# Kernel tuning notes

Measured on AMD Instinct MI355X. Metric: run time of the kernel, lower is better.

The kernel has to match this reference:

```python
import jax, jax.numpy as jnp
import numpy as np


def setup_inputs() -> dict:
    key = jax.random.key(0)
    ks = jax.random.split(key, 16)
    N, F_in, C, E = 50000, 128, 64, 800000
    H = 2 * C      # hidden width of first GCN layer = 128
    P = 128        # num_proj_hidden
    K = 3          # cluster_num (hardcoded in GRACE)

    def lin(kw, fan_in, fan_out):
        # torch Linear default init: U(-1/sqrt(fan_in), 1/sqrt(fan_in))
        bound = 1.0 / np.sqrt(fan_in)
        return jax.random.uniform(kw, (fan_in, fan_out), jnp.float32, -bound, bound)

    inp = {
        "x1": jax.random.normal(ks[0], (N, F_in), jnp.float32),
        "edge_index1": jax.random.randint(ks[1], (2, E), 0, N, jnp.int64 if jax.config.jax_enable_x64 else jnp.int32),
        "x2": jax.random.normal(ks[2], (N, F_in), jnp.float32),
        "edge_index2": jax.random.randint(ks[3], (2, E), 0, N, jnp.int64 if jax.config.jax_enable_x64 else jnp.int32),
        # encoder GCN layers
        "W1": lin(ks[4], F_in, H), "b1": jnp.zeros((H,), jnp.float32),
        "W2": lin(ks[5], H, C),    "b2": jnp.zeros((C,), jnp.float32),
        # instance projector: Linear(C,C) -> ReLU -> Linear(C,P)
        "Wp1": lin(ks[6], C, C), "bp1": jnp.zeros((C,), jnp.float32),
        "Wp2": lin(ks[7], C, P), "bp2": jnp.zeros((P,), jnp.float32),
        # cluster projector: Linear(C,C) -> ReLU -> Linear(C,K) -> Softmax
        "Wc1": lin(ks[8], C, C), "bc1": jnp.zeros((C,), jnp.float32),
        "Wc2": lin(ks[9], C, K), "bc2": jnp.zeros((K,), jnp.float32),
    }
    return inp


def _gcn_encoder(x, edge_index, W1, b1, W2, b2):
    N = x.shape[0]
    loop = jnp.arange(N, dtype=edge_index.dtype)
    row = jnp.concatenate([edge_index[0], loop])  # message sources (x_j)
    col = jnp.concatenate([edge_index[1], loop])  # aggregation targets
    deg = jax.ops.segment_sum(jnp.ones_like(col, jnp.float32), col, num_segments=N)
    dinv = jax.lax.rsqrt(deg)  # deg >= 1 due to self loops
    norm = dinv[row] * dinv[col]  # [E+N]

    def layer(h, W, b):
        h = h @ W  # transform first (PyG GCNConv), [N, F_out]
        msg = h[row] * norm[:, None]  # gather + scale, [E+N, F_out]
        return jax.ops.segment_sum(msg, col, num_segments=N) + b

    h = jax.nn.relu(layer(x, W1, b1))
    h = jax.nn.relu(layer(h, W2, b2))
    return h


def _l2norm(z, eps=1e-12):
    # matches F.normalize(z, dim=1): x / max(||x||, eps)
    n = jnp.sqrt(jnp.sum(z * z, axis=1, keepdims=True))
    return z / jnp.maximum(n, eps)


def reference(x1, edge_index1, x2, edge_index2,
              W1, b1, W2, b2, Wp1, bp1, Wp2, bp2, Wc1, bc1, Wc2, bc2):
    z1 = _gcn_encoder(x1, edge_index1, W1, b1, W2, b2)
    z2 = _gcn_encoder(x2, edge_index2, W1, b1, W2, b2)

    inst = lambda z: _l2norm(jax.nn.relu(z @ Wp1 + bp1) @ Wp2 + bp2)
    clus = lambda z: jax.nn.softmax(jax.nn.relu(z @ Wc1 + bc1) @ Wc2 + bc2, axis=1)

    z_i = inst(z1)
    z_j = inst(z2)
    c_i = clus(z1)
    c_j = clus(z2)
    return (z_i, z_j, c_i, c_j)
```

## Files before the change

### kernel.cpp

```cpp
#include <hip/hip_runtime.h>
#include <cstdint>
#include <cstddef>

using u16 = unsigned short;
using u32 = unsigned int;

typedef __bf16 bf16x8 __attribute__((ext_vector_type(8)));
typedef float  f32x4  __attribute__((ext_vector_type(4)));

__device__ __forceinline__ float bf2f(u16 b) { union { u32 i; float f; } v; v.i = ((u32)b) << 16; return v.f; }
__device__ __forceinline__ u16 f2bf(float f) { __bf16 b = (__bf16)f; return __builtin_bit_cast(u16, b); }
__device__ __forceinline__ float bflo(u32 u) { union { u32 i; float f; } v; v.i = u << 16; return v.f; }
__device__ __forceinline__ float bfhi(u32 u) { union { u32 i; float f; } v; v.i = u & 0xffff0000u; return v.f; }
__device__ __forceinline__ u32 pack2(float a, float b) { return (u32)f2bf(a) | ((u32)f2bf(b) << 16); }

__device__ __forceinline__ float loadx(const void* p, size_t i, int flag_bf16) {
    return flag_bf16 ? bf2f(((const u16*)p)[i]) : ((const float*)p)[i];
}
__device__ __forceinline__ void storex(void* p, size_t i, float v, int flag_bf16) {
    if (flag_bf16) ((u16*)p)[i] = f2bf(v);
    else           ((float*)p)[i] = v;
}

__device__ __forceinline__ bf16x8 load_afrag_ext(const void* A, size_t off, int flag) {
    if (flag) return *reinterpret_cast<const bf16x8*>((const u16*)A + off);
    const float* f = (const float*)A + off;
    float4 a = *reinterpret_cast<const float4*>(f);
    float4 b = *reinterpret_cast<const float4*>(f + 4);
    bf16x8 r;
    r[0] = (__bf16)a.x; r[1] = (__bf16)a.y; r[2] = (__bf16)a.z; r[3] = (__bf16)a.w;
    r[4] = (__bf16)b.x; r[5] = (__bf16)b.y; r[6] = (__bf16)b.z; r[7] = (__bf16)b.w;
    return r;
}

__global__ void k_detect(const u32* __restrict__ x, int* __restrict__ flag) {
    int lane = threadIdx.x;
    u32 u = x[lane];
    int e = (u >> 7) & 0xFF;
    int hit = (e >= 100 && e <= 145) ? 1 : 0;
    unsigned long long b = __ballot(hit);
    if (lane == 0) flag[0] = (__popcll(b) >= 32) ? 1 : 0;
}

struct ConvJob { const void* src; float* dst; int n; };
struct ConvJobs { ConvJob j[12]; };

__global__ void k_wconv(ConvJobs jobs, const int* __restrict__ flagp) {
    const int f = *flagp;
    const int stride = gridDim.x * blockDim.x;
    for (int s = 0; s < 12; ++s) {
        const ConvJob jb = jobs.j[s];
        for (int i = blockIdx.x * blockDim.x + threadIdx.x; i < jb.n; i += stride)
            jb.dst[i] = loadx(jb.src, i, f);
    }
}

struct TJob { const float* W; u16* WT; int K, NC; };
struct TJobs { TJob j[5]; };

__global__ void k_wtrans(TJobs jobs) {
    const int stride = gridDim.x * blockDim.x;
    for (int s = 0; s < 5; ++s) {
        const TJob jb = jobs.j[s];
        const int tot = jb.K * jb.NC;
        for (int i = blockIdx.x * blockDim.x + threadIdx.x; i < tot; i += stride) {
            int k = i / jb.NC, n = i - k * jb.NC;
            jb.WT[n * jb.K + k] = f2bf(jb.W[i]);
        }
    }
}

static const int CAPSH = 12;
static const int OVCAP = 65536;

__global__ __launch_bounds__(256) void k_bin(const int* __restrict__ ei0, const int* __restrict__ ei1,
                                             int* __restrict__ cur, u32* __restrict__ stage,
                                             int2* __restrict__ ov, int* __restrict__ ocnt,
                                             int E, int NB, int nblk) {
    const int g = blockIdx.y;
    const int* ei = g ? ei1 : ei0;
    const int chunk = (E + nblk - 1) / nblk;
    const int e0 = blockIdx.x * chunk;
    const int e1 = (e0 + chunk < E) ? e0 + chunk : E;
    const int tid = threadIdx.x;
    __shared__ int h[512];
    __shared__ int lb[512];
    for (int i = tid; i < NB; i += 256) h[i] = 0;
    __syncthreads();
    for (int e = e0 + tid; e < e1; e += 256) {
        int d = __builtin_nontemporal_load(ei + E + e);
        atomicAdd(&h[d >> 7], 1);
    }
    __syncthreads();
    for (int b = tid; b < NB; b += 256) {
        int c = h[b];
        lb[b] = c ? atomicAdd(&cur[g * NB + b], c) : 0;
    }
    __syncthreads();
    for (int i = tid; i < NB; i += 256) h[i] = 0;
    __syncthreads();
    for (int e = e0 + tid; e < e1; e += 256) {
        int s = __builtin_nontemporal_load(ei + e);
        int d = ei[E + e];
        int b = d >> 7;
        int p = lb[b] + atomicAdd(&h[b], 1);
        if (p < (1 << CAPSH)) {
            stage[((size_t)(g * NB + b) << CAPSH) + p] = (u32)s | ((u32)(d & 127) << 16);
        } else {
            int oi = atomicAdd(ocnt, 1);
            if (oi < OVCAP) ov[oi] = make_int2(s, d | (g << 24));
        }
    }
}

__global__ __launch_bounds__(256) void k_bscan(const int* __restrict__ cur, const int2* __restrict__ ov,
                                               const int* __restrict__ ocnt, int* __restrict__ bbase,
                                               int* __restrict__ rowptr, int N, int E, int NB) {
    __shared__ int tot[2][512];
    const int tid = threadIdx.x;
    for (int g = 0; g < 2; ++g)
        for (int i = tid; i < 512; i += 256) {
            int s = 0;
            if (i < NB) {
                int cv = cur[g * NB + i];
                s = (cv < (1 << CAPSH)) ? cv : (1 << CAPSH);
            }
            tot[g][i] = s;
        }
    __syncthreads();
    int no = *ocnt; if (no > OVCAP) no = OVCAP;
    for (int i = tid; i < no; i += 256) {
        int y = ov[i].y;
        atomicAdd(&tot[y >> 24][(y & 0xFFFFFF) >> 7], 1);
    }
    __syncthreads();
    int o00 = tot[0][tid], o01 = tot[0][tid + 256];
    int o10 = tot[1][tid], o11 = tot[1][tid + 256];
    for (int off = 1; off < 512; off <<= 1) {
        int a0 = tot[0][tid]       + ((tid >= off)       ? tot[0][tid - off]       : 0);
        int a1 = tot[0][tid + 256] + ((tid + 256 >= off) ? tot[0][tid + 256 - off] : 0);
        int b0 = tot[1][tid]       + ((tid >= off)       ? tot[1][tid - off]       : 0);
        int b1 = tot[1][tid + 256] + ((tid + 256 >= off) ? tot[1][tid + 256 - off] : 0);
        __syncthreads();
        tot[0][tid] = a0; tot[0][tid + 256] = a1;
        tot[1][tid] = b0; tot[1][tid + 256] = b1;
        __syncthreads();
    }
    if (tid < NB)       { bbase[tid]            = tot[0][tid] - o00;       bbase[NB + tid]       = tot[1][tid] - o10; }
    if (tid + 256 < NB) { bbase[tid + 256]      = tot[0][tid + 256] - o01; bbase[NB + tid + 256] = tot[1][tid + 256] - o11; }
    if (tid == 0) {
        rowptr[N] = E;
        rowptr[(size_t)(N + 1) + N] = E;
    }
}

__global__ __launch_bounds__(256) void k_scatter(const int* __restrict__ cur, const u32* __restrict__ stage,
                                                 const int2* __restrict__ ov, const int* __restrict__ ocnt,
                                                 const int* __restrict__ bbase, int* __restrict__ rowptr,
                                                 float* __restrict__ dinv, int* __restrict__ csr,
                                                 int N, int E, int NB) {
    const int g = blockIdx.y, b = blockIdx.x, tid = threadIdx.x;
    const int lo = b << 7;
    int R = N - lo; if (R > 128) R = 128;
    __shared__ int hist[128], scn[128], curs[128];
    if (tid < 128) hist[tid] = 0;
    __syncthreads();
    int cv = cur[g * NB + b];
    const int n = (cv < (1 << CAPSH)) ? cv : (1 << CAPSH);
    const u32* sp = stage + ((size_t)(g * NB + b) << CAPSH);
    for (int i = tid; i < n; i += 256) atomicAdd(&hist[sp[i] >> 16], 1);
    int no = *ocnt; if (no > OVCAP) no = OVCAP;
    for (int i = tid; i < no; i += 256) {
        int y = ov[i].y;
        if ((y >> 24) != g) continue;
        int d = y & 0xFFFFFF;
        if (d >= lo && d < lo + 128) atomicAdd(&hist[d - lo], 1);
    }
    __syncthreads();
    int orig = (tid < 128) ? hist[tid] : 0;
    if (tid < 128) scn[tid] = orig;
    __syncthreads();
    for (int off = 1; off < 128; off <<= 1) {
        int v = 0;
        if (tid < 128) v = scn[tid] + ((tid >= off) ? scn[tid - off] : 0);
        __syncthreads();
        if (tid < 128) scn[tid] = v;
        __syncthreads();
    }
    const int base = bbase[g * NB + b];
    if (tid < R) {
        int ex = base + scn[tid] - orig;
        rowptr[(size_t)g * (N + 1) + lo + tid] = ex;
        curs[tid] = ex;
        dinv[(size_t)g * N + lo + tid] = rsqrtf((float)(orig + 1));
    }
    __syncthreads();
    int* out = csr + (size_t)g * E;
    for (int i = tid; i < n; i += 256) {
        u32 v = sp[i];
        int pos = atomicAdd(&curs[v >> 16], 1);
        out[pos] = (int)(v & 0xFFFFu);
    }
    for (int i = tid; i < no; i += 256) {
        int y = ov[i].y;
        if ((y >> 24) != g) continue;
        int d = y & 0xFFFFFF;
        if (d >= lo && d < lo + 128) {
            int pos = atomicAdd(&curs[d - lo], 1);
            out[pos] = ov[i].x;
        }
    }
}

template <int K, int NC, bool AEXT, bool BIAS, bool RELU, bool NORM, bool OEXT, bool SCALE>
__global__ __launch_bounds__(256) void k_mgemm(const void* __restrict__ A0, const void* __restrict__ A1,
                                               size_t astride, const u16* __restrict__ WT,
                                               const float* __restrict__ bias, void* __restrict__ outv,
                                               size_t out_off, size_t ostride, int M,
                                               const int* __restrict__ flagp,
                                               const float* __restrict__ dvp) {
    constexpr int NT = NC / 16;
    constexpr int KI = K / 32;
    const int flag = *flagp;
    const int g = blockIdx.y;
    const void* Av = g ? A1 : A0;
    const int lane = threadIdx.x & 63;
    const int wave = threadIdx.x >> 6;
    const int q = lane >> 4;
    const int c = lane & 15;
    const int m0 = blockIdx.x * 64 + wave * 16;
    int arow = m0 + c;
    if (arow > M - 1) arow = M - 1;
    const size_t abase = (size_t)g * astride + (size_t)arow * K;

    bf16x8 afr[KI];
#pragma unroll
    for (int ki = 0; ki < KI; ++ki) {
        size_t off = abase + (size_t)ki * 32 + q * 8;
        if (AEXT) afr[ki] = load_afrag_ext(Av, off, flag);
        else      afr[ki] = *reinterpret_cast<const bf16x8*>((const u16*)Av + off);
    }

    f32x4 acc[NT];
#pragma unroll
    for (int t = 0; t < NT; ++t) acc[t] = (f32x4){0.f, 0.f, 0.f, 0.f};

#pragma unroll
    for (int ki = 0; ki < KI; ++ki) {
#pragma unroll
        for (int t = 0; t < NT; ++t) {
            const u16* bptr = WT + (size_t)(t * 16 + c) * K + ki * 32 + q * 8;
            bf16x8 bfr = *reinterpret_cast<const bf16x8*>(bptr);
            acc[t] = __builtin_amdgcn_mfma_f32_16x16x32_bf16(afr[ki], bfr, acc[t], 0, 0, 0);
        }
    }

#pragma unroll
    for (int t = 0; t < NT; ++t) {
        float bv = BIAS ? bias[t * 16 + c] : 0.f;
#pragma unroll
        for (int r = 0; r < 4; ++r) {
            float v = acc[t][r] + bv;
            if (RELU) v = fmaxf(v, 0.f);
            acc[t][r] = v;
        }
    }

    if constexpr (NORM) {
        float ss[4] = {0.f, 0.f, 0.f, 0.f};
#pragma unroll
        for (int t = 0; t < NT; ++t)
#pragma unroll
            for (int r = 0; r < 4; ++r) ss[r] += acc[t][r] * acc[t][r];
#pragma unroll
        for (int r = 0; r < 4; ++r) {
#pragma unroll
            for (int m = 1; m < 16; m <<= 1) ss[r] += __shfl_xor(ss[r], m, 64);
            float s = 1.f / fmaxf(sqrtf(ss[r]), 1e-12f);
#pragma unroll
            for (int t = 0; t < NT; ++t) acc[t][r] *= s;
        }
    }

    const size_t obase = out_off + (size_t)g * ostride;
#pragma unroll
    for (int r = 0; r < 4; ++r) {
        const int grow = m0 + q * 4 + r;
        if (grow < M) {
            float sc = 1.f;
            if constexpr (SCALE) sc = dvp[(size_t)g * M + grow];
#pragma unroll
            for (int t = 0; t < NT; ++t) {
                float v = SCALE ? acc[t][r] * sc : acc[t][r];
                size_t oi = obase + (size_t)grow * NC + t * 16 + c;
                if (OEXT) storex(outv, oi, v, flag);
                else      ((u16*)outv)[oi] = f2bf(v);
            }
        }
    }
}

__global__ __launch_bounds__(256) void k_agg128(const u32* __restrict__ H, const int* __restrict__ rowptr,
                                                const int* __restrict__ csr, const float* __restrict__ dinv,
                                                const float* __restrict__ bias, u32* __restrict__ out,
                                                int N, int E) {
    const int g = blockIdx.y;
    const int node = blockIdx.x * 4 + (threadIdx.x >> 6);
    if (node >= N) return;
    const int lane = threadIdx.x & 63;
    const u32* h = H + (size_t)g * N * 64;
    const int* rp = rowptr + (size_t)g * (N + 1);
    const int* cs = csr + (size_t)g * E;
    const float dn = dinv[(size_t)g * N + node];
    int e = rp[node];
    const int end = rp[node + 1];
    u32 su = h[(size_t)node * 64 + lane];
    float a0 = bflo(su), a1 = bfhi(su);
    while (e < end) {
        int cnt = end - e; if (cnt > 64) cnt = 64;
        int my = (lane < cnt) ? cs[e + lane] : 0;
        int j = 0;
        for (; j + 8 <= cnt; j += 8) {
            int sx[8];
#pragma unroll
            for (int k = 0; k < 8; ++k) sx[k] = __shfl(my, j + k, 64);
            u32 hv[8];
#pragma unroll
            for (int k = 0; k < 8; ++k) hv[k] = h[(size_t)sx[k] * 64 + lane];
#pragma unroll
            for (int k = 0; k < 8; ++k) { a0 += bflo(hv[k]); a1 += bfhi(hv[k]); }
        }
        for (; j < cnt; ++j) {
            int s = __shfl(my, j, 64);
            u32 hv = h[(size_t)s * 64 + lane];
            a0 += bflo(hv); a1 += bfhi(hv);
        }
        e += cnt;
    }
    a0 = fmaxf(a0 * dn + bias[2 * lane], 0.f);
    a1 = fmaxf(a1 * dn + bias[2 * lane + 1], 0.f);
    out[((size_t)g * N + node) * 64 + lane] = pack2(a0, a1);
}

__global__ __launch_bounds__(256) void k_agg64(const u16* __restrict__ H, const int* __restrict__ rowptr,
                                               const int* __restrict__ csr, const float* __restrict__ dinv,
                                               const float* __restrict__ bias, u16* __restrict__ out,
                                               int N, int E) {
    const int g = blockIdx.y;
    const int node = blockIdx.x * 4 + (threadIdx.x >> 6);
    if (node >= N) return;
    const int lane = threadIdx.x & 63;
    const u16* h = H + (size_t)g * N * 64;
    const int* rp = rowptr + (size_t)g * (N + 1);
    const int* cs = csr + (size_t)g * E;
    const float dn = dinv[(size_t)g * N + node];
    int e = rp[node];
    const int end = rp[node + 1];
    float a0 = bf2f(h[(size_t)node * 64 + lane]);
    while (e < end) {
        int cnt = end - e; if (cnt > 64) cnt = 64;
        int my = (lane < cnt) ? cs[e + lane] : 0;
        int j = 0;
        for (; j + 8 <= cnt; j += 8) {
            int sx[8];
#pragma unroll
            for (int k = 0; k < 8; ++k) sx[k] = __shfl(my, j + k, 64);
            u16 hv[8];
#pragma unroll
            for (int k = 0; k < 8; ++k) hv[k] = h[(size_t)sx[k] * 64 + lane];
#pragma unroll
            for (int k = 0; k < 8; ++k) a0 += bf2f(hv[k]);
        }
        for (; j < cnt; ++j) {
            int s = __shfl(my, j, 64);
            a0 += bf2f(h[(size_t)s * 64 + lane]);
        }
        e += cnt;
    }
    a0 = fmaxf(a0 * dn + bias[lane], 0.f);
    out[((size_t)g * N + node) * 64 + lane] = f2bf(a0);
}

__global__ __launch_bounds__(256) void k_clus(const u16* __restrict__ v, const float* __restrict__ Wc2,
                                              const float* __restrict__ bc2, void* __restrict__ outv,
                                              size_t out_off, size_t ostride, int N,
                                              const int* __restrict__ flagp) {
    const int g = blockIdx.y;
    const int node = blockIdx.x * 4 + (threadIdx.x >> 6);
    if (node >= N) return;
    const int flag = *flagp;
    const int lane = threadIdx.x & 63;
    float ul = bf2f(v[((size_t)g * N + node) * 64 + lane]);
    float a0 = ul * Wc2[lane * 3 + 0];
    float a1 = ul * Wc2[lane * 3 + 1];
    float a2 = ul * Wc2[lane * 3 + 2];
#pragma unroll
    for (int m = 1; m < 64; m <<= 1) {
        a0 += __shfl_xor(a0, m, 64);
        a1 += __shfl_xor(a1, m, 64);
        a2 += __shfl_xor(a2, m, 64);
    }
    a0 += bc2[0]; a1 += bc2[1]; a2 += bc2[2];
    float mx = fmaxf(a0, fmaxf(a1, a2));
    float e0 = expf(a0 - mx), e1 = expf(a1 - mx), e2 = expf(a2 - mx);
    float inv = 1.f / (e0 + e1 + e2);
    if (lane < 3) {
        float r = (lane == 0) ? e0 : ((lane == 1) ? e1 : e2);
        storex(outv, out_off + (size_t)g * ostride + (size_t)node * 3 + lane, r * inv, flag);
    }
}

extern "C" void kernel_launch(void* const* d_in, const int* in_sizes, int n_in,
                              void* d_out, int out_size, void* d_ws, size_t ws_size,
                              hipStream_t stream) {
    const int N = in_sizes[0] / 128;
    const int E = in_sizes[1] / 2;
    const int* ei0 = (const int*)d_in[1];
    const int* ei1 = (const int*)d_in[3];
    const int NB = (N + 127) >> 7;

    size_t off = 0;
    auto alloc = [&](size_t bytes) -> void* {
        void* p = (char*)d_ws + off;
        off += (bytes + 255) & ~(size_t)255;
        return p;
    };
    int* flag = (int*)alloc(256);
    const int wcnt[12] = {128 * 128, 128, 128 * 64, 64, 64 * 64, 64, 64 * 128, 128, 64 * 64, 64, 64 * 3, 3};
    float* wf[12];
    for (int i = 0; i < 12; ++i) wf[i] = (float*)alloc((size_t)wcnt[i] * 4);
    float* b1f = wf[1]; float* b2f = wf[3]; float* bp1f = wf[5]; float* bp2f = wf[7];
    float* bc1f = wf[9]; float* Wc2f = wf[10]; float* bc2f = wf[11];
    u16* W1T  = (u16*)alloc(128 * 128 * 2);
    u16* W2T  = (u16*)alloc(64 * 128 * 2);
    u16* Wp1T = (u16*)alloc(64 * 64 * 2);
    u16* Wp2T = (u16*)alloc(128 * 64 * 2);
    u16* Wc1T = (u16*)alloc(64 * 64 * 2);

    const int ncell = 2 * NB;
    int* cur    = (int*)alloc((size_t)(ncell + 1) * 4);
    int* ocnt   = cur + ncell;
    int2* ov    = (int2*)alloc((size_t)OVCAP * 8);
    u32* stage  = (u32*)alloc(((size_t)ncell << CAPSH) * 4);
    int* bbase  = (int*)alloc((size_t)2 * NB * 4);
    int* rowptr = (int*)alloc((size_t)2 * (N + 1) * 4);
    float* dinv = (float*)alloc((size_t)2 * N * 4);
    int* csr    = (int*)alloc((size_t)2 * E * 4);
    u16* A1 = (u16*)alloc((size_t)2 * N * 128 * 2);
    u16* H2 = A1;
    u16* Qb = (u16*)alloc((size_t)2 * N * 128 * 2);
    u16* U  = Qb;
    u16* Z  = (u16*)alloc((size_t)2 * N * 64 * 2);
    (void)ws_size; (void)n_in; (void)out_size;

    k_detect<<<1, 64, 0, stream>>>((const u32*)d_in[0], flag);
    ConvJobs jobs;
    for (int i = 0; i < 12; ++i) jobs.j[i] = ConvJob{d_in[4 + i], wf[i], wcnt[i]};
    k_wconv<<<64, 256, 0, stream>>>(jobs, flag);
    TJobs tj;
    tj.j[0] = TJob{wf[0], W1T, 128, 128};
    tj.j[1] = TJob{wf[2], W2T, 128, 64};
    tj.j[2] = TJob{wf[4], Wp1T, 64, 64};
    tj.j[3] = TJob{wf[6], Wp2T, 64, 128};
    tj.j[4] = TJob{wf[8], Wc1T, 64, 64};
    k_wtrans<<<40, 256, 0, stream>>>(tj);

    hipMemsetAsync(cur, 0, (size_t)(ncell + 1) * 4, stream);
    const int NBLK = 128;
    k_bin<<<dim3(NBLK, 2), 256, 0, stream>>>(ei0, ei1, cur, stage, ov, ocnt, E, NB, NBLK);
    k_bscan<<<1, 256, 0, stream>>>(cur, ov, ocnt, bbase, rowptr, N, E, NB);
    k_scatter<<<dim3(NB, 2), 256, 0, stream>>>(cur, stage, ov, ocnt, bbase, rowptr, dinv, csr, N, E, NB);

    const dim3 gM((N + 63) / 64, 2);
    const dim3 gA((N + 3) / 4, 2);

    k_mgemm<128, 128, true, false, false, false, false, true><<<gM, 256, 0, stream>>>(
        d_in[0], d_in[2], 0, W1T, nullptr, A1, 0, (size_t)N * 128, N, flag, dinv);
    k_agg128<<<gA, 256, 0, stream>>>((const u32*)A1, rowptr, csr, dinv, b1f, (u32*)Qb, N, E);
    k_mgemm<128, 64, false, false, false, false, false, true><<<gM, 256, 0, stream>>>(
        Qb, Qb, (size_t)N * 128, W2T, nullptr, H2, 0, (size_t)N * 64, N, flag, dinv);
    k_agg64<<<gA, 256, 0, stream>>>(H2, rowptr, csr, dinv, b2f, Z, N, E);

    k_mgemm<64, 64, false, true, true, false, false, false><<<gM, 256, 0, stream>>>(
        Z, Z, (size_t)N * 64, Wp1T, bp1f, U, 0, (size_t)N * 64, N, flag, nullptr);
    k_mgemm<64, 128, false, true, false, true, true, false><<<gM, 256, 0, stream>>>(
        U, U, (size_t)N * 64, Wp2T, bp2f, d_out, 0, (size_t)N * 128, N, flag, nullptr);
    k_mgemm<64, 64, false, true, true, false, false, false><<<gM, 256, 0, stream>>>(
        Z, Z, (size_t)N * 64, Wc1T, bc1f, U, 0, (size_t)N * 64, N, flag, nullptr);
    k_clus<<<gA, 256, 0, stream>>>(U, Wc2f, bc2f, d_out,
                                   (size_t)2 * N * 128, (size_t)N * 3, N, flag);
}
```

Before: 423.8 us.

## Split node features into column slabs for cache-friendly GCN aggregation

Node feature matrices are stored as per-graph column slabs (32 or 16 bf16 channels per slab, 64 or 32 bytes per row) instead of full-width rows. The aggregation kernels now interleave graph and slab in the block index, so consecutive blocks gather from one small slab that fits better in L2. Each wave splits its lanes into groups that process several edges at once and combine results with cross-lane shuffles. In exchange each gathered row segment is narrower, neighbor indices are re-read once per slab, and the GEMM kernels gain strided slab indexing for inputs and outputs.

```diff
diff --git a/kernel.cpp b/kernel.cpp
--- a/kernel.cpp
+++ b/kernel.cpp
@@ -212,7 +212,8 @@
     }
 }
 
-template <int K, int NC, bool AEXT, bool BIAS, bool RELU, bool NORM, bool OEXT, bool SCALE>
+template <int K, int NC, bool AEXT, bool BIAS, bool RELU, bool NORM, bool OEXT, bool SCALE,
+          int ASPLIT, int OSPLIT>
 __global__ __launch_bounds__(256) void k_mgemm(const void* __restrict__ A0, const void* __restrict__ A1,
                                                size_t astride, const u16* __restrict__ WT,
                                                const float* __restrict__ bias, void* __restrict__ outv,
@@ -223,7 +224,7 @@
     constexpr int KI = K / 32;
     const int flag = *flagp;
     const int g = blockIdx.y;
-    const void* Av = g ? A1 : A0;
+    const void* Av = (ASPLIT != 0) ? A0 : (g ? A1 : A0);
     const int lane = threadIdx.x & 63;
     const int wave = threadIdx.x >> 6;
     const int q = lane >> 4;
@@ -236,7 +237,14 @@
     bf16x8 afr[KI];
 #pragma unroll
     for (int ki = 0; ki < KI; ++ki) {
-        size_t off = abase + (size_t)ki * 32 + q * 8;
+        size_t off;
+        if constexpr (ASPLIT == 32) {
+            off = ((size_t)(g * (K / 32) + ki)) * ((size_t)M * 32) + (size_t)arow * 32 + q * 8;
+        } else if constexpr (ASPLIT == 16) {
+            off = ((size_t)(g * (K / 16) + ki * 2 + (q >> 1))) * ((size_t)M * 16) + (size_t)arow * 16 + (q & 1) * 8;
+        } else {
+            off = abase + (size_t)ki * 32 + q * 8;
+        }
         if (AEXT) afr[ki] = load_afrag_ext(Av, off, flag);
         else      afr[ki] = *reinterpret_cast<const bf16x8*>((const u16*)Av + off);
     }
@@ -292,9 +300,18 @@
 #pragma unroll
             for (int t = 0; t < NT; ++t) {
                 float v = SCALE ? acc[t][r] * sc : acc[t][r];
-                size_t oi = obase + (size_t)grow * NC + t * 16 + c;
-                if (OEXT) storex(outv, oi, v, flag);
-                else      ((u16*)outv)[oi] = f2bf(v);
+                const int ch = t * 16 + c;
+                if constexpr (OSPLIT == 32) {
+                    size_t oi = ((size_t)(g * (NC / 32) + (ch >> 5))) * ((size_t)M * 32) + (size_t)grow * 32 + (ch & 31);
+                    ((u16*)outv)[oi] = f2bf(v);
+                } else if constexpr (OSPLIT == 16) {
+                    size_t oi = ((size_t)(g * (NC / 16) + (ch >> 4))) * ((size_t)M * 16) + (size_t)grow * 16 + (ch & 15);
+                    ((u16*)outv)[oi] = f2bf(v);
+                } else {
+                    size_t oi = obase + (size_t)grow * NC + ch;
+                    if (OEXT) storex(outv, oi, v, flag);
+                    else      ((u16*)outv)[oi] = f2bf(v);
+                }
             }
         }
     }
@@ -304,81 +321,130 @@
                                                 const int* __restrict__ csr, const float* __restrict__ dinv,
                                                 const float* __restrict__ bias, u32* __restrict__ out,
                                                 int N, int E) {
-    const int g = blockIdx.y;
-    const int node = blockIdx.x * 4 + (threadIdx.x >> 6);
-    if (node >= N) return;
+    const int bid = blockIdx.x;
+    const int g = (bid >> 2) & 1;
+    const int q = bid & 3;
+    const int nb = bid >> 3;
     const int lane = threadIdx.x & 63;
-    const u32* h = H + (size_t)g * N * 64;
+    const int wv = threadIdx.x >> 6;
+    const int grp = lane >> 4;
+    const int w = lane & 15;
+    const u32* h = H + (size_t)(g * 4 + q) * N * 16;
     const int* rp = rowptr + (size_t)g * (N + 1);
     const int* cs = csr + (size_t)g * E;
-    const float dn = dinv[(size_t)g * N + node];
-    int e = rp[node];
-    const int end = rp[node + 1];
-    u32 su = h[(size_t)node * 64 + lane];
-    float a0 = bflo(su), a1 = bfhi(su);
-    while (e < end) {
-        int cnt = end - e; if (cnt > 64) cnt = 64;
-        int my = (lane < cnt) ? cs[e + lane] : 0;
-        int j = 0;
-        for (; j + 8 <= cnt; j += 8) {
-            int sx[8];
-#pragma unroll
-            for (int k = 0; k < 8; ++k) sx[k] = __shfl(my, j + k, 64);
-            u32 hv[8];
-#pragma unroll
-            for (int k = 0; k < 8; ++k) hv[k] = h[(size_t)sx[k] * 64 + lane];
-#pragma unroll
-            for (int k = 0; k < 8; ++k) { a0 += bflo(hv[k]); a1 += bfhi(hv[k]); }
-        }
-        for (; j < cnt; ++j) {
-            int s = __shfl(my, j, 64);
-            u32 hv = h[(size_t)s * 64 + lane];
-            a0 += bflo(hv); a1 += bfhi(hv);
-        }
-        e += cnt;
-    }
-    a0 = fmaxf(a0 * dn + bias[2 * lane], 0.f);
-    a1 = fmaxf(a1 * dn + bias[2 * lane + 1], 0.f);
-    out[((size_t)g * N + node) * 64 + lane] = pack2(a0, a1);
-}
-
-__global__ __launch_bounds__(256) void k_agg64(const u16* __restrict__ H, const int* __restrict__ rowptr,
+    u32* o = out + (size_t)(g * 4 + q) * N * 16;
+#pragma unroll
+    for (int i = 0; i < 2; ++i) {
+        const int node = nb * 8 + wv * 2 + i;
+        if (node >= N) return;
+        int e = rp[node];
+        const int end = rp[node + 1];
+        u32 su = (grp == 0) ? h[(size_t)node * 16 + w] : 0u;
+        float a0 = bflo(su), a1 = bfhi(su);
+        while (e < end) {
+            int cnt = end - e; if (cnt > 64) cnt = 64;
+            int my = (lane < cnt) ? cs[e + lane] : 0;
+            int j = 0;
+            for (; j + 16 <= cnt; j += 16) {
+                int s0 = __shfl(my, j + grp, 64);
+                int s1 = __shfl(my, j + 4 + grp, 64);
+                int s2 = __shfl(my, j + 8 + grp, 64);
+                int s3 = __shfl(my, j + 12 + grp, 64);
+                u32 h0 = h[(size_t)s0 * 16 + w];
+                u32 h1 = h[(size_t)s1 * 16 + w];
+                u32 h2 = h[(size_t)s2 * 16 + w];
+                u32 h3 = h[(size_t)s3 * 16 + w];
+                a0 += bflo(h0); a1 += bfhi(h0);
+                a0 += bflo(h1); a1 += bfhi(h1);
+                a0 += bflo(h2); a1 += bfhi(h2);
+                a0 += bflo(h3); a1 += bfhi(h3);
+            }
+            for (; j < cnt; j += 4) {
+                int idx = j + grp;
+                int src = __shfl(my, idx < cnt ? idx : 0, 64);
+                if (idx < cnt) {
+                    u32 hv = h[(size_t)src * 16 + w];
+                    a0 += bflo(hv); a1 += bfhi(hv);
+                }
+            }
+            e += cnt;
+        }
+        a0 += __shfl_xor(a0, 16, 64); a0 += __shfl_xor(a0, 32, 64);
+        a1 += __shfl_xor(a1, 16, 64); a1 += __shfl_xor(a1, 32, 64);
+        if (grp == 0) {
+            float dn = dinv[(size_t)g * N + node];
+            float b0 = bias[q * 32 + 2 * w];
+            float b1 = bias[q * 32 + 2 * w + 1];
+            float r0 = fmaxf(a0 * dn + b0, 0.f);
+            float r1 = fmaxf(a1 * dn + b1, 0.f);
+            o[(size_t)node * 16 + w] = pack2(r0, r1);
+        }
+    }
+}
+
+__global__ __launch_bounds__(256) void k_agg64(const u32* __restrict__ H, const int* __restrict__ rowptr,
                                                const int* __restrict__ csr, const float* __restrict__ dinv,
-                                               const float* __restrict__ bias, u16* __restrict__ out,
+                                               const float* __restrict__ bias, u32* __restrict__ out,
                                                int N, int E) {
-    const int g = blockIdx.y;
-    const int node = blockIdx.x * 4 + (threadIdx.x >> 6);
-    if (node >= N) return;
+    const int bid = blockIdx.x;
+    const int g = (bid >> 2) & 1;
+    const int q = bid & 3;
+    const int nb = bid >> 3;
     const int lane = threadIdx.x & 63;
-    const u16* h = H + (size_t)g * N * 64;
+    const int wv = threadIdx.x >> 6;
+    const int grp = lane >> 3;
+    const int w = lane & 7;
+    const u32* h = H + (size_t)(g * 4 + q) * N * 8;
     const int* rp = rowptr + (size_t)g * (N + 1);
     const int* cs = csr + (size_t)g * E;
-    const float dn = dinv[(size_t)g * N + node];
-    int e = rp[node];
-    const int end = rp[node + 1];
-    float a0 = bf2f(h[(size_t)node * 64 + lane]);
-    while (e < end) {
-        int cnt = end - e; if (cnt > 64) cnt = 64;
-        int my = (lane < cnt) ? cs[e + lane] : 0;
-        int j = 0;
-        for (; j + 8 <= cnt; j += 8) {
-            int sx[8];
-#pragma unroll
-            for (int k = 0; k < 8; ++k) sx[k] = __shfl(my, j + k, 64);
-            u16 hv[8];
-#pragma unroll
-            for (int k = 0; k < 8; ++k) hv[k] = h[(size_t)sx[k] * 64 + lane];
-#pragma unroll
-            for (int k = 0; k < 8; ++k) a0 += bf2f(hv[k]);
-        }
-        for (; j < cnt; ++j) {
-            int s = __shfl(my, j, 64);
-            a0 += bf2f(h[(size_t)s * 64 + lane]);
-        }
-        e += cnt;
-    }
-    a0 = fmaxf(a0 * dn + bias[lane], 0.f);
-    out[((size_t)g * N + node) * 64 + lane] = f2bf(a0);
+    u32* o = out + (size_t)(g * 4 + q) * N * 8;
+#pragma unroll
+    for (int i = 0; i < 2; ++i) {
+        const int node = nb * 8 + wv * 2 + i;
+        if (node >= N) return;
+        int e = rp[node];
+        const int end = rp[node + 1];
+        u32 su = (grp == 0) ? h[(size_t)node * 8 + w] : 0u;
+        float a0 = bflo(su), a1 = bfhi(su);
+        while (e < end) {
+            int cnt = end - e; if (cnt > 64) cnt = 64;
+            int my = (lane < cnt) ? cs[e + lane] : 0;
+            int j = 0;
+            for (; j + 32 <= cnt; j += 32) {
+                int s0 = __shfl(my, j + grp, 64);
+                int s1 = __shfl(my, j + 8 + grp, 64);
+                int s2 = __shfl(my, j + 16 + grp, 64);
+                int s3 = __shfl(my, j + 24 + grp, 64);
+                u32 h0 = h[(size_t)s0 * 8 + w];
+                u32 h1 = h[(size_t)s1 * 8 + w];
+                u32 h2 = h[(size_t)s2 * 8 + w];
+                u32 h3 = h[(size_t)s3 * 8 + w];
+                a0 += bflo(h0); a1 += bfhi(h0);
+                a0 += bflo(h1); a1 += bfhi(h1);
+                a0 += bflo(h2); a1 += bfhi(h2);
+                a0 += bflo(h3); a1 += bfhi(h3);
+            }
+            for (; j < cnt; j += 8) {
+                int idx = j + grp;
+                int src = __shfl(my, idx < cnt ? idx : 0, 64);
+                if (idx < cnt) {
+                    u32 hv = h[(size_t)src * 8 + w];
+                    a0 += bflo(hv); a1 += bfhi(hv);
+                }
+            }
+            e += cnt;
+        }
+        a0 += __shfl_xor(a0, 8, 64); a0 += __shfl_xor(a0, 16, 64); a0 += __shfl_xor(a0, 32, 64);
+        a1 += __shfl_xor(a1, 8, 64); a1 += __shfl_xor(a1, 16, 64); a1 += __shfl_xor(a1, 32, 64);
+        if (grp == 0) {
+            float dn = dinv[(size_t)g * N + node];
+            float b0 = bias[q * 16 + 2 * w];
+            float b1 = bias[q * 16 + 2 * w + 1];
+            float r0 = fmaxf(a0 * dn + b0, 0.f);
+            float r1 = fmaxf(a1 * dn + b1, 0.f);
+            o[(size_t)node * 8 + w] = pack2(r0, r1);
+        }
+    }
 }
 
 __global__ __launch_bounds__(256) void k_clus(const u16* __restrict__ v, const float* __restrict__ Wc2,
@@ -472,21 +538,22 @@
     k_scatter<<<dim3(NB, 2), 256, 0, stream>>>(cur, stage, ov, ocnt, bbase, rowptr, dinv, csr, N, E, NB);
 
     const dim3 gM((N + 63) / 64, 2);
+    const dim3 gAg(8 * ((N + 7) / 8));
     const dim3 gA((N + 3) / 4, 2);
 
-    k_mgemm<128, 128, true, false, false, false, false, true><<<gM, 256, 0, stream>>>(
+    k_mgemm<128, 128, true, false, false, false, false, true, 0, 32><<<gM, 256, 0, stream>>>(
         d_in[0], d_in[2], 0, W1T, nullptr, A1, 0, (size_t)N * 128, N, flag, dinv);
-    k_agg128<<<gA, 256, 0, stream>>>((const u32*)A1, rowptr, csr, dinv, b1f, (u32*)Qb, N, E);
-    k_mgemm<128, 64, false, false, false, false, false, true><<<gM, 256, 0, stream>>>(
-        Qb, Qb, (size_t)N * 128, W2T, nullptr, H2, 0, (size_t)N * 64, N, flag, dinv);
-    k_agg64<<<gA, 256, 0, stream>>>(H2, rowptr, csr, dinv, b2f, Z, N, E);
-
-    k_mgemm<64, 64, false, true, true, false, false, false><<<gM, 256, 0, stream>>>(
-        Z, Z, (size_t)N * 64, Wp1T, bp1f, U, 0, (size_t)N * 64, N, flag, nullptr);
-    k_mgemm<64, 128, false, true, false, true, true, false><<<gM, 256, 0, stream>>>(
+    k_agg128<<<gAg, 256, 0, stream>>>((const u32*)A1, rowptr, csr, dinv, b1f, (u32*)Qb, N, E);
+    k_mgemm<128, 64, false, false, false, false, false, true, 32, 16><<<gM, 256, 0, stream>>>(
+        Qb, Qb, 0, W2T, nullptr, H2, 0, (size_t)N * 64, N, flag, dinv);
+    k_agg64<<<gAg, 256, 0, stream>>>((const u32*)H2, rowptr, csr, dinv, b2f, (u32*)Z, N, E);
+
+    k_mgemm<64, 64, false, true, true, false, false, false, 16, 0><<<gM, 256, 0, stream>>>(
+        Z, Z, 0, Wp1T, bp1f, U, 0, (size_t)N * 64, N, flag, nullptr);
+    k_mgemm<64, 128, false, true, false, true, true, false, 0, 0><<<gM, 256, 0, stream>>>(
         U, U, (size_t)N * 64, Wp2T, bp2f, d_out, 0, (size_t)N * 128, N, flag, nullptr);
-    k_mgemm<64, 64, false, true, true, false, false, false><<<gM, 256, 0, stream>>>(
-        Z, Z, (size_t)N * 64, Wc1T, bc1f, U, 0, (size_t)N * 64, N, flag, nullptr);
+    k_mgemm<64, 64, false, true, true, false, false, false, 16, 0><<<gM, 256, 0, stream>>>(
+        Z, Z, 0, Wc1T, bc1f, U, 0, (size_t)N * 64, N, flag, nullptr);
     k_clus<<<gA, 256, 0, stream>>>(U, Wc2f, bc2f, d_out,
                                    (size_t)2 * N * 128, (size_t)N * 3, N, flag);
 }
```

Result: slower. 512.3 us (+20.9%).
